# Kernel tuning notes

Measured on AMD Instinct MI355X. Metric: run time of the kernel, lower is better.

Reference implementation:

```python
import jax, jax.numpy as jnp
import numpy as np

SEARCH_RANGE = 4


def setup_inputs() -> dict:
    key = jax.random.key(0)
    k1, k2 = jax.random.split(key)
    B, C, H, W = 4, 64, 256, 256
    x1 = jax.random.normal(k1, (B, C, H, W), dtype=jnp.float32)
    x2 = jax.random.normal(k2, (B, C, H, W), dtype=jnp.float32)
    return {"x1": x1, "x2": x2}


def reference(x1, x2):
    r = SEARCH_RANGE
    D = (2 * r + 1) ** 2
    B, C, H, W = x1.shape
    # zero-pad x2 so out-of-range correlations contribute 0 (matches the
    # original, which leaves those cv entries at their zero init)
    x2p = jnp.pad(x2, ((0, 0), (0, 0), (r, r), (r, r)))
    chans = [None] * D
    for i in range(-r, r + 1):
        for j in range(-r, r + 1):
            # torch cv[:, (2r+1)*i + j] wraps negative indices -> mod D
            k = ((2 * r + 1) * i + j) % D
            # x2 sample at (h - i, w - j): window of padded x2
            win = jax.lax.dynamic_slice(
                x2p, (0, 0, r - i, r - j), (B, C, H, W))
            chans[k] = jnp.sum(x1 * win, axis=1)  # [B,H,W]
    cv = jnp.stack(chans, axis=1)  # [B,D,H,W]
    return jax.nn.softmax(cv, axis=1)  # alpha=1, raw_output=False
```

## Files before the change

### kernel.cpp

```cpp
#include <hip/hip_runtime.h>
#include <stddef.h>

namespace {
constexpr int Hc = 256, Wc = 256, Cc = 64, Bc = 4, Dc = 81;
constexpr int CH = Hc * Wc;
}

#define PIN() asm volatile("" ::: "memory")
#define VMW(N) asm volatile("s_waitcnt vmcnt(" #N ")" ::: "memory")

#define DPPL(x) __builtin_amdgcn_update_dpp(0, (x), 0x138, 0xf, 0xf, true)
#define DPPR(x) __builtin_amdgcn_update_dpp(0, (x), 0x130, 0xf, 0xf, true)

typedef __fp16 half2v __attribute__((ext_vector_type(2)));

static __device__ __forceinline__ int pk2(float a, float b) {
#if __has_builtin(__builtin_amdgcn_cvt_pkrtz)
    half2v h = __builtin_amdgcn_cvt_pkrtz(a, b);
#else
    half2v h; h.x = (__fp16)a; h.y = (__fp16)b;
#endif
    return __builtin_bit_cast(int, h);
}

static __device__ __forceinline__ float dot2f(int q, int w, float c) {
#if __has_builtin(__builtin_amdgcn_fdot2)
    return __builtin_amdgcn_fdot2(__builtin_bit_cast(half2v, q),
                                  __builtin_bit_cast(half2v, w), c, false);
#else
    half2v a = __builtin_bit_cast(half2v, q);
    half2v b = __builtin_bit_cast(half2v, w);
    return c + (float)a.x * (float)b.x + (float)a.y * (float)b.y;
#endif
}

#define FMP(A0, A1, XI)                                                     \
    do {                                                                    \
        const int P0_ = pk2(A0.x, A1.x), P1_ = pk2(A0.y, A1.y);             \
        const int P2_ = pk2(A0.z, A1.z), P3_ = pk2(A0.w, A1.w);             \
        const int w_[12] = {DPPL(P0_), DPPL(P1_), DPPL(P2_), DPPL(P3_),     \
                            P0_,       P1_,       P2_,       P3_,           \
                            DPPR(P0_), DPPR(P1_), DPPR(P2_), DPPR(P3_)};    \
        const int q_[4] = {XI.x, XI.y, XI.z, XI.w};                         \
        _Pragma("unroll") for (int jj = 0; jj < 9; ++jj)                    \
            _Pragma("unroll") for (int s = 0; s < 4; ++s)                   \
                acc[jj][s] = dot2f(q_[s], w_[s - jj + 8], acc[jj][s]);      \
    } while (0)

#define ISX(T, OFF)                                                         \
    do {                                                                    \
        xq##T = *(const float4*)(x2p + (size_t)(OFF) * CH);                 \
        PIN();                                                              \
    } while (0)

#define RX1(X, IDX) X = *(const int4*)&xp[(IDX) * 256 + 4 * t]

__global__ __launch_bounds__(576)
void corr_softmax_kernel(const float* __restrict__ x1,
                         const float* __restrict__ x2,
                         float* __restrict__ out)
{
    __shared__ __align__(16) int xp[32 * 256];

    const int tid = threadIdx.x;
    const int wi  = tid >> 6;
    const int t   = tid & 63;
    const int bid = blockIdx.x;
    const int bh  = (bid & 7) * 128 + (bid >> 3);
    const int b   = bh >> 8;
    const int h   = bh & 255;

    const float* x1row = x1 + (size_t)b * Cc * CH + (size_t)h * Wc;
#pragma unroll
    for (int kk = 0; kk < 4; ++kk) {
        const int T = tid + 576 * kk;
        if (T < 2048) {
            const int e = T >> 6, p = T & 63;
            float4 a0 = *(const float4*)(x1row + (size_t)(2 * e) * CH + 4 * p);
            float4 a1 = *(const float4*)(x1row + (size_t)(2 * e + 1) * CH + 4 * p);
            int4 w;
            w.x = pk2(a0.x, a1.x); w.y = pk2(a0.y, a1.y);
            w.z = pk2(a0.z, a1.z); w.w = pk2(a0.w, a1.w);
            *(int4*)&xp[e * 256 + 4 * p] = w;
        }
    }
    __syncthreads();

    float acc[9][4];
#pragma unroll
    for (int jj = 0; jj < 9; ++jj)
#pragma unroll
        for (int s = 0; s < 4; ++s)
            acc[jj][s] = 0.f;

    const int r  = h + 4 - wi;
    const int rr = (r < 0) ? 0 : ((r > 255) ? 255 : r);

    const float* x2p = x2 + (size_t)b * Cc * CH + (size_t)rr * Wc + 4 * t;

    float4 xq0, xq1, xq2, xq3, xq4, xq5, xq6, xq7;
    int4 xa, xb;

    ISX(0, 0); ISX(1, 1); ISX(2, 2); ISX(3, 3);
    ISX(4, 4); ISX(5, 5); ISX(6, 6); ISX(7, 7);
    RX1(xa, 0);

#pragma unroll 1
    for (int g = 0; g < 7; ++g) {
        const int e1 = 4 * g;
        VMW(6); RX1(xb, e1 + 1); FMP(xq0, xq1, xa); ISX(0, 8);  ISX(1, 9);
        VMW(6); RX1(xa, e1 + 2); FMP(xq2, xq3, xb); ISX(2, 10); ISX(3, 11);
        VMW(6); RX1(xb, e1 + 3); FMP(xq4, xq5, xa); ISX(4, 12); ISX(5, 13);
        VMW(6); RX1(xa, e1 + 4); FMP(xq6, xq7, xb); ISX(6, 14); ISX(7, 15);
        x2p += (size_t)8 * CH;
    }
    VMW(6); RX1(xb, 29); FMP(xq0, xq1, xa);
    VMW(4); RX1(xa, 30); FMP(xq2, xq3, xb);
    VMW(2); RX1(xb, 31); FMP(xq4, xq5, xa);
    VMW(0); FMP(xq6, xq7, xb);

    if ((unsigned)r >= (unsigned)Hc) {
#pragma unroll
        for (int jj = 0; jj < 9; ++jj)
#pragma unroll
            for (int s = 0; s < 4; ++s)
                acc[jj][s] = 0.f;
    }

    __syncthreads();
    float* red = (float*)xp;

    float m0, m1, m2, m3;
    {
        float v0 = acc[0][0], v1 = acc[0][1], v2 = acc[0][2], v3 = acc[0][3];
#pragma unroll
        for (int jj = 1; jj < 9; ++jj) {
            v0 = fmaxf(v0, acc[jj][0]);
            v1 = fmaxf(v1, acc[jj][1]);
            v2 = fmaxf(v2, acc[jj][2]);
            v3 = fmaxf(v3, acc[jj][3]);
        }
        m0 = v0; m1 = v1; m2 = v2; m3 = v3;
    }
    *(float4*)(red + wi * 256 + 4 * t) = make_float4(m0, m1, m2, m3);
    __syncthreads();

    float M0, M1, M2, M3;
    {
        float4 q = *(const float4*)(red + 4 * t);
        M0 = q.x; M1 = q.y; M2 = q.z; M3 = q.w;
#pragma unroll
        for (int w2 = 1; w2 < 9; ++w2) {
            float4 qq = *(const float4*)(red + w2 * 256 + 4 * t);
            M0 = fmaxf(M0, qq.x); M1 = fmaxf(M1, qq.y);
            M2 = fmaxf(M2, qq.z); M3 = fmaxf(M3, qq.w);
        }
    }

    float s0 = 0.f, s1 = 0.f, s2 = 0.f, s3 = 0.f;
#pragma unroll
    for (int jj = 0; jj < 9; ++jj) {
        acc[jj][0] = __expf(acc[jj][0] - M0); s0 += acc[jj][0];
        acc[jj][1] = __expf(acc[jj][1] - M1); s1 += acc[jj][1];
        acc[jj][2] = __expf(acc[jj][2] - M2); s2 += acc[jj][2];
        acc[jj][3] = __expf(acc[jj][3] - M3); s3 += acc[jj][3];
    }
    __syncthreads();
    *(float4*)(red + wi * 256 + 4 * t) = make_float4(s0, s1, s2, s3);
    __syncthreads();

    float S0, S1, S2, S3;
    {
        float4 q = *(const float4*)(red + 4 * t);
        S0 = q.x; S1 = q.y; S2 = q.z; S3 = q.w;
#pragma unroll
        for (int w2 = 1; w2 < 9; ++w2) {
            float4 qq = *(const float4*)(red + w2 * 256 + 4 * t);
            S0 += qq.x; S1 += qq.y; S2 += qq.z; S3 += qq.w;
        }
    }
    const float i0 = 1.0f / S0, i1 = 1.0f / S1, i2 = 1.0f / S2, i3 = 1.0f / S3;

    float* outp = out + (size_t)b * Dc * CH + (size_t)h * Wc + 4 * t;
#pragma unroll
    for (int jj = 0; jj < 9; ++jj) {
        int kc = 9 * wi + jj + 41;
        if (kc >= 81) kc -= 81;
        float4 o = make_float4(acc[jj][0] * i0, acc[jj][1] * i1,
                               acc[jj][2] * i2, acc[jj][3] * i3);
        *(float4*)(outp + (size_t)kc * CH) = o;
    }
}

extern "C" void kernel_launch(void* const* d_in, const int* in_sizes, int n_in,
                              void* d_out, int out_size, void* d_ws, size_t ws_size,
                              hipStream_t stream) {
    (void)in_sizes; (void)n_in; (void)d_ws; (void)ws_size; (void)out_size;
    const float* x1 = (const float*)d_in[0];
    const float* x2 = (const float*)d_in[1];
    float* out = (float*)d_out;
    dim3 grid(Bc * Hc);
    dim3 block(576);
    hipLaunchKernelGGL(corr_softmax_kernel, grid, block, 0, stream, x1, x2, out);
}
```

Baseline: 77.14 us.

## Split each row across two blocks and channel halves per wave with halo exchange

```diff
diff --git a/kernel.cpp b/kernel.cpp
--- a/kernel.cpp
+++ b/kernel.cpp
@@ -8,6 +8,7 @@
 
 #define PIN() asm volatile("" ::: "memory")
 #define VMW(N) asm volatile("s_waitcnt vmcnt(" #N ")" ::: "memory")
+#define LGK(N) asm volatile("s_waitcnt lgkmcnt(" #N ")" ::: "memory")
 
 #define DPPL(x) __builtin_amdgcn_update_dpp(0, (x), 0x138, 0xf, 0xf, true)
 #define DPPR(x) __builtin_amdgcn_update_dpp(0, (x), 0x130, 0xf, 0xf, true)
@@ -34,54 +35,134 @@
 #endif
 }
 
-#define FMP(A0, A1, XI)                                                     \
+#define FMPx(A0, A1, XI, SM, LS)                                            \
     do {                                                                    \
         const int P0_ = pk2(A0.x, A1.x), P1_ = pk2(A0.y, A1.y);             \
         const int P2_ = pk2(A0.z, A1.z), P3_ = pk2(A0.w, A1.w);             \
-        const int w_[12] = {DPPL(P0_), DPPL(P1_), DPPL(P2_), DPPL(P3_),     \
-                            P0_,       P1_,       P2_,       P3_,           \
-                            DPPR(P0_), DPPR(P1_), DPPR(P2_), DPPR(P3_)};    \
+        int l0_ = DPPL(P0_), l1_ = DPPL(P1_);                               \
+        int l2_ = DPPL(P2_), l3_ = DPPL(P3_);                               \
+        int r0_ = DPPR(P0_), r1_ = DPPR(P1_);                               \
+        int r2_ = DPPR(P2_), r3_ = DPPR(P3_);                               \
+        if (LS) {                                                           \
+            l0_ = c0 ? SM.x : l0_; l1_ = c0 ? SM.y : l1_;                   \
+            l2_ = c0 ? SM.z : l2_; l3_ = c0 ? SM.w : l3_;                   \
+            r0_ = c31 ? 0 : r0_;  r1_ = c31 ? 0 : r1_;                      \
+            r2_ = c31 ? 0 : r2_;  r3_ = c31 ? 0 : r3_;                      \
+        } else {                                                            \
+            l0_ = c0 ? 0 : l0_;  l1_ = c0 ? 0 : l1_;                        \
+            l2_ = c0 ? 0 : l2_;  l3_ = c0 ? 0 : l3_;                        \
+            r0_ = c31 ? SM.x : r0_; r1_ = c31 ? SM.y : r1_;                 \
+            r2_ = c31 ? SM.z : r2_; r3_ = c31 ? SM.w : r3_;                 \
+        }                                                                   \
+        const int w_[12] = {l0_, l1_, l2_, l3_, P0_, P1_, P2_, P3_,         \
+                            r0_, r1_, r2_, r3_};                            \
         const int q_[4] = {XI.x, XI.y, XI.z, XI.w};                         \
         _Pragma("unroll") for (int jj = 0; jj < 9; ++jj)                    \
             _Pragma("unroll") for (int s = 0; s < 4; ++s)                   \
                 acc[jj][s] = dot2f(q_[s], w_[s - jj + 8], acc[jj][s]);      \
     } while (0)
 
-#define ISX(T, OFF)                                                         \
-    do {                                                                    \
-        xq##T = *(const float4*)(x2p + (size_t)(OFF) * CH);                 \
+#define STEPF(Qa, Qb, XC, SC, XN, SN, E2, OA, OB, LS)                       \
+    do {                                                                    \
+        VMW(6);                                                             \
+        XN = *(const int4*)&xp[(hb + (E2)) * 128 + 4 * tl];                 \
+        SN = *(const int4*)&smk[4 * (wi * 32 + hb + (E2))];                 \
+        LGK(4);                                                             \
+        FMPx(Qa, Qb, XC, SC, LS);                                           \
+        Qa = *(const float4*)(x2p + (size_t)(OA) * CH);                     \
+        Qb = *(const float4*)(x2p + (size_t)(OB) * CH);                     \
         PIN();                                                              \
     } while (0)
 
-#define RX1(X, IDX) X = *(const int4*)&xp[(IDX) * 256 + 4 * t]
+#define STEPD(Qa, Qb, XC, SC, XN, SN, E2, VN, LS)                           \
+    do {                                                                    \
+        VMW(VN);                                                            \
+        XN = *(const int4*)&xp[(hb + (E2)) * 128 + 4 * tl];                 \
+        SN = *(const int4*)&smk[4 * (wi * 32 + hb + (E2))];                 \
+        LGK(4);                                                             \
+        FMPx(Qa, Qb, XC, SC, LS);                                           \
+    } while (0)
+
+#define STEPZ(Qa, Qb, XC, SC, VN, LN, LS)                                   \
+    do { VMW(VN); LGK(LN); FMPx(Qa, Qb, XC, SC, LS); } while (0)
+
+#define MAINLOOP(LS)                                                        \
+    do {                                                                    \
+        STEPF(xq0, xq1, xiA, smA, xiC, smC, 2, 8, 9, LS);                   \
+        STEPF(xq2, xq3, xiB, smB, xiA, smA, 3, 10, 11, LS);                 \
+        STEPF(xq4, xq5, xiC, smC, xiB, smB, 4, 12, 13, LS);                 \
+        STEPF(xq6, xq7, xiA, smA, xiC, smC, 5, 14, 15, LS);                 \
+        x2p += (size_t)8 * CH;                                              \
+        STEPF(xq0, xq1, xiB, smB, xiA, smA, 6, 8, 9, LS);                   \
+        STEPF(xq2, xq3, xiC, smC, xiB, smB, 7, 10, 11, LS);                 \
+        STEPF(xq4, xq5, xiA, smA, xiC, smC, 8, 12, 13, LS);                 \
+        STEPF(xq6, xq7, xiB, smB, xiA, smA, 9, 14, 15, LS);                 \
+        x2p += (size_t)8 * CH;                                              \
+        STEPF(xq0, xq1, xiC, smC, xiB, smB, 10, 8, 9, LS);                  \
+        STEPF(xq2, xq3, xiA, smA, xiC, smC, 11, 10, 11, LS);                \
+        STEPF(xq4, xq5, xiB, smB, xiA, smA, 12, 12, 13, LS);                \
+        STEPF(xq6, xq7, xiC, smC, xiB, smB, 13, 14, 15, LS);                \
+        x2p += (size_t)8 * CH;                                              \
+        STEPD(xq0, xq1, xiA, smA, xiC, smC, 14, 6, LS);                     \
+        STEPD(xq2, xq3, xiB, smB, xiA, smA, 15, 4, LS);                     \
+        STEPZ(xq4, xq5, xiC, smC, 2, 2, LS);                                \
+        STEPZ(xq6, xq7, xiA, smA, 0, 0, LS);                                \
+    } while (0)
 
 __global__ __launch_bounds__(576)
 void corr_softmax_kernel(const float* __restrict__ x1,
                          const float* __restrict__ x2,
                          float* __restrict__ out)
 {
-    __shared__ __align__(16) int xp[32 * 256];
-
-    const int tid = threadIdx.x;
-    const int wi  = tid >> 6;
-    const int t   = tid & 63;
+    __shared__ __align__(16) int xp[32 * 128];
+    __shared__ __align__(16) int smk[9 * 32 * 4];
+
+    const int tid  = threadIdx.x;
+    const int wi   = tid >> 6;
+    const int t    = tid & 63;
+    const int half = t >> 5;
+    const int tl   = t & 31;
+    const int hb   = 16 * half;
+    const bool c0  = (tl == 0), c31 = (tl == 31);
+
     const int bid = blockIdx.x;
-    const int bh  = (bid & 7) * 128 + (bid >> 3);
-    const int b   = bh >> 8;
-    const int h   = bh & 255;
-
-    const float* x1row = x1 + (size_t)b * Cc * CH + (size_t)h * Wc;
-#pragma unroll
-    for (int kk = 0; kk < 4; ++kk) {
+    const int u   = (bid & 7) * 256 + (bid >> 3);
+    const int b   = u >> 9;
+    const int rem = u & 511;
+    const int h   = rem >> 1;
+    const int hw  = rem & 1;
+
+    const int r  = h + 4 - wi;
+    const int rr = (r < 0) ? 0 : ((r > 255) ? 255 : r);
+
+    const float* x1row = x1 + (size_t)b * Cc * CH + (size_t)h * Wc + 128 * hw;
+#pragma unroll
+    for (int kk = 0; kk < 2; ++kk) {
         const int T = tid + 576 * kk;
-        if (T < 2048) {
-            const int e = T >> 6, p = T & 63;
+        if (T < 1024) {
+            const int e = T >> 5, p = T & 31;
             float4 a0 = *(const float4*)(x1row + (size_t)(2 * e) * CH + 4 * p);
-            float4 a1 = *(const float4*)(x1row + (size_t)(2 * e + 1) * CH + 4 * p);
+            float4 a1 = *(const float4*)(x1row + (size_t)(2 * e) * CH + CH + 4 * p);
             int4 w;
             w.x = pk2(a0.x, a1.x); w.y = pk2(a0.y, a1.y);
             w.z = pk2(a0.z, a1.z); w.w = pk2(a0.w, a1.w);
-            *(int4*)&xp[e * 256 + 4 * p] = w;
+            *(int4*)&xp[e * 128 + 4 * p] = w;
+        }
+    }
+
+    {
+        const int sb = hw ? 124 : 128;
+        const float* sp = x2 + (size_t)b * Cc * CH + (size_t)t * CH
+                        + (size_t)rr * Wc + sb;
+        float4 sv = *(const float4*)sp;
+        float4 pv;
+        pv.x = __shfl_xor(sv.x, 1); pv.y = __shfl_xor(sv.y, 1);
+        pv.z = __shfl_xor(sv.z, 1); pv.w = __shfl_xor(sv.w, 1);
+        if ((t & 1) == 0) {
+            int4 w;
+            w.x = pk2(sv.x, pv.x); w.y = pk2(sv.y, pv.y);
+            w.z = pk2(sv.z, pv.z); w.w = pk2(sv.w, pv.w);
+            *(int4*)&smk[4 * (wi * 32 + (t >> 1))] = w;
         }
     }
     __syncthreads();
@@ -93,31 +174,27 @@
         for (int s = 0; s < 4; ++s)
             acc[jj][s] = 0.f;
 
-    const int r  = h + 4 - wi;
-    const int rr = (r < 0) ? 0 : ((r > 255) ? 255 : r);
-
-    const float* x2p = x2 + (size_t)b * Cc * CH + (size_t)rr * Wc + 4 * t;
+    const float* x2p = x2 + (size_t)b * Cc * CH + (size_t)(32 * half) * CH
+                     + (size_t)rr * Wc + 128 * hw + 4 * tl;
 
     float4 xq0, xq1, xq2, xq3, xq4, xq5, xq6, xq7;
-    int4 xa, xb;
-
-    ISX(0, 0); ISX(1, 1); ISX(2, 2); ISX(3, 3);
-    ISX(4, 4); ISX(5, 5); ISX(6, 6); ISX(7, 7);
-    RX1(xa, 0);
-
-#pragma unroll 1
-    for (int g = 0; g < 7; ++g) {
-        const int e1 = 4 * g;
-        VMW(6); RX1(xb, e1 + 1); FMP(xq0, xq1, xa); ISX(0, 8);  ISX(1, 9);
-        VMW(6); RX1(xa, e1 + 2); FMP(xq2, xq3, xb); ISX(2, 10); ISX(3, 11);
-        VMW(6); RX1(xb, e1 + 3); FMP(xq4, xq5, xa); ISX(4, 12); ISX(5, 13);
-        VMW(6); RX1(xa, e1 + 4); FMP(xq6, xq7, xb); ISX(6, 14); ISX(7, 15);
-        x2p += (size_t)8 * CH;
-    }
-    VMW(6); RX1(xb, 29); FMP(xq0, xq1, xa);
-    VMW(4); RX1(xa, 30); FMP(xq2, xq3, xb);
-    VMW(2); RX1(xb, 31); FMP(xq4, xq5, xa);
-    VMW(0); FMP(xq6, xq7, xb);
+    int4 xiA, xiB, xiC, smA, smB, smC;
+
+    xiA = *(const int4*)&xp[(hb + 0) * 128 + 4 * tl];
+    smA = *(const int4*)&smk[4 * (wi * 32 + hb + 0)];
+    xiB = *(const int4*)&xp[(hb + 1) * 128 + 4 * tl];
+    smB = *(const int4*)&smk[4 * (wi * 32 + hb + 1)];
+    xq0 = *(const float4*)(x2p + (size_t)0 * CH);
+    xq1 = *(const float4*)(x2p + (size_t)1 * CH);
+    xq2 = *(const float4*)(x2p + (size_t)2 * CH);
+    xq3 = *(const float4*)(x2p + (size_t)3 * CH);
+    xq4 = *(const float4*)(x2p + (size_t)4 * CH);
+    xq5 = *(const float4*)(x2p + (size_t)5 * CH);
+    xq6 = *(const float4*)(x2p + (size_t)6 * CH);
+    xq7 = *(const float4*)(x2p + (size_t)7 * CH);
+    PIN();
+
+    if (hw == 0) { MAINLOOP(0); } else { MAINLOOP(1); }
 
     if ((unsigned)r >= (unsigned)Hc) {
 #pragma unroll
@@ -126,6 +203,12 @@
             for (int s = 0; s < 4; ++s)
                 acc[jj][s] = 0.f;
     }
+
+#pragma unroll
+    for (int jj = 0; jj < 9; ++jj)
+#pragma unroll
+        for (int s = 0; s < 4; ++s)
+            acc[jj][s] += __shfl_xor(acc[jj][s], 32);
 
     __syncthreads();
     float* red = (float*)xp;
@@ -142,16 +225,17 @@
         }
         m0 = v0; m1 = v1; m2 = v2; m3 = v3;
     }
-    *(float4*)(red + wi * 256 + 4 * t) = make_float4(m0, m1, m2, m3);
+    if (half == 0)
+        *(float4*)(red + wi * 128 + 4 * tl) = make_float4(m0, m1, m2, m3);
     __syncthreads();
 
     float M0, M1, M2, M3;
     {
-        float4 q = *(const float4*)(red + 4 * t);
+        float4 q = *(const float4*)(red + 4 * tl);
         M0 = q.x; M1 = q.y; M2 = q.z; M3 = q.w;
 #pragma unroll
         for (int w2 = 1; w2 < 9; ++w2) {
-            float4 qq = *(const float4*)(red + w2 * 256 + 4 * t);
+            float4 qq = *(const float4*)(red + w2 * 128 + 4 * tl);
             M0 = fmaxf(M0, qq.x); M1 = fmaxf(M1, qq.y);
             M2 = fmaxf(M2, qq.z); M3 = fmaxf(M3, qq.w);
         }
@@ -166,29 +250,33 @@
         acc[jj][3] = __expf(acc[jj][3] - M3); s3 += acc[jj][3];
     }
     __syncthreads();
-    *(float4*)(red + wi * 256 + 4 * t) = make_float4(s0, s1, s2, s3);
+    if (half == 0)
+        *(float4*)(red + wi * 128 + 4 * tl) = make_float4(s0, s1, s2, s3);
     __syncthreads();
 
     float S0, S1, S2, S3;
     {
-        float4 q = *(const float4*)(red + 4 * t);
+        float4 q = *(const float4*)(red + 4 * tl);
         S0 = q.x; S1 = q.y; S2 = q.z; S3 = q.w;
 #pragma unroll
         for (int w2 = 1; w2 < 9; ++w2) {
-            float4 qq = *(const float4*)(red + w2 * 256 + 4 * t);
+            float4 qq = *(const float4*)(red + w2 * 128 + 4 * tl);
             S0 += qq.x; S1 += qq.y; S2 += qq.z; S3 += qq.w;
         }
     }
     const float i0 = 1.0f / S0, i1 = 1.0f / S1, i2 = 1.0f / S2, i3 = 1.0f / S3;
 
-    float* outp = out + (size_t)b * Dc * CH + (size_t)h * Wc + 4 * t;
-#pragma unroll
-    for (int jj = 0; jj < 9; ++jj) {
-        int kc = 9 * wi + jj + 41;
-        if (kc >= 81) kc -= 81;
-        float4 o = make_float4(acc[jj][0] * i0, acc[jj][1] * i1,
-                               acc[jj][2] * i2, acc[jj][3] * i3);
-        *(float4*)(outp + (size_t)kc * CH) = o;
+    if (half == 0) {
+        float* outp = out + (size_t)b * Dc * CH + (size_t)h * Wc
+                    + 128 * hw + 4 * tl;
+#pragma unroll
+        for (int jj = 0; jj < 9; ++jj) {
+            int kc = 9 * wi + jj + 41;
+            if (kc >= 81) kc -= 81;
+            float4 o = make_float4(acc[jj][0] * i0, acc[jj][1] * i1,
+                                   acc[jj][2] * i2, acc[jj][3] * i3);
+            *(float4*)(outp + (size_t)kc * CH) = o;
+        }
     }
 }
 
@@ -199,7 +287,7 @@
     const float* x1 = (const float*)d_in[0];
     const float* x2 = (const float*)d_in[1];
     float* out = (float*)d_out;
-    dim3 grid(Bc * Hc);
+    dim3 grid(2048);
     dim3 block(576);
     hipLaunchKernelGGL(corr_softmax_kernel, grid, block, 0, stream, x1, x2, out);
 }
```

Result: slower. 98.58 us (+27.8%).

## Process four rows per block with persistent grid and prefetch next x1 row

Applied to the files above, without the earlier changes.

```diff
diff --git a/kernel.cpp b/kernel.cpp
--- a/kernel.cpp
+++ b/kernel.cpp
@@ -55,140 +55,155 @@
 
 #define RX1(X, IDX) X = *(const int4*)&xp[(IDX) * 256 + 4 * t]
 
+#define STAGE_X1(BB, HH)                                                    \
+    do {                                                                    \
+        const float* x1row_ = x1 + (size_t)(BB) * Cc * CH + (size_t)(HH) * Wc; \
+        _Pragma("unroll")                                                   \
+        for (int kk = 0; kk < 4; ++kk) {                                    \
+            const int T = tid + 576 * kk;                                   \
+            if (T < 2048) {                                                 \
+                const int e = T >> 6, p = T & 63;                           \
+                float4 a0 = *(const float4*)(x1row_ + (size_t)(2 * e) * CH + 4 * p); \
+                float4 a1 = *(const float4*)(x1row_ + (size_t)(2 * e + 1) * CH + 4 * p); \
+                int4 w;                                                     \
+                w.x = pk2(a0.x, a1.x); w.y = pk2(a0.y, a1.y);               \
+                w.z = pk2(a0.z, a1.z); w.w = pk2(a0.w, a1.w);               \
+                *(int4*)&xp[e * 256 + 4 * p] = w;                           \
+            }                                                               \
+        }                                                                   \
+    } while (0)
+
 __global__ __launch_bounds__(576)
 void corr_softmax_kernel(const float* __restrict__ x1,
                          const float* __restrict__ x2,
                          float* __restrict__ out)
 {
-    __shared__ __align__(16) int xp[32 * 256];
+    __shared__ __align__(16) int   xp[32 * 256];
+    __shared__ __align__(16) float red[9 * 256];
 
     const int tid = threadIdx.x;
     const int wi  = tid >> 6;
     const int t   = tid & 63;
-    const int bid = blockIdx.x;
-    const int bh  = (bid & 7) * 128 + (bid >> 3);
-    const int b   = bh >> 8;
-    const int h   = bh & 255;
-
-    const float* x1row = x1 + (size_t)b * Cc * CH + (size_t)h * Wc;
-#pragma unroll
-    for (int kk = 0; kk < 4; ++kk) {
-        const int T = tid + 576 * kk;
-        if (T < 2048) {
-            const int e = T >> 6, p = T & 63;
-            float4 a0 = *(const float4*)(x1row + (size_t)(2 * e) * CH + 4 * p);
-            float4 a1 = *(const float4*)(x1row + (size_t)(2 * e + 1) * CH + 4 * p);
-            int4 w;
-            w.x = pk2(a0.x, a1.x); w.y = pk2(a0.y, a1.y);
-            w.z = pk2(a0.z, a1.z); w.w = pk2(a0.w, a1.w);
-            *(int4*)&xp[e * 256 + 4 * p] = w;
-        }
-    }
+    const int bid  = blockIdx.x;
+    const int base = (bid & 7) * 128 + (bid >> 3) * 4;
+
+    STAGE_X1(base >> 8, base & 255);
     __syncthreads();
 
-    float acc[9][4];
-#pragma unroll
-    for (int jj = 0; jj < 9; ++jj)
-#pragma unroll
-        for (int s = 0; s < 4; ++s)
-            acc[jj][s] = 0.f;
-
-    const int r  = h + 4 - wi;
-    const int rr = (r < 0) ? 0 : ((r > 255) ? 255 : r);
-
-    const float* x2p = x2 + (size_t)b * Cc * CH + (size_t)rr * Wc + 4 * t;
-
-    float4 xq0, xq1, xq2, xq3, xq4, xq5, xq6, xq7;
-    int4 xa, xb;
-
-    ISX(0, 0); ISX(1, 1); ISX(2, 2); ISX(3, 3);
-    ISX(4, 4); ISX(5, 5); ISX(6, 6); ISX(7, 7);
-    RX1(xa, 0);
-
 #pragma unroll 1
-    for (int g = 0; g < 7; ++g) {
-        const int e1 = 4 * g;
-        VMW(6); RX1(xb, e1 + 1); FMP(xq0, xq1, xa); ISX(0, 8);  ISX(1, 9);
-        VMW(6); RX1(xa, e1 + 2); FMP(xq2, xq3, xb); ISX(2, 10); ISX(3, 11);
-        VMW(6); RX1(xb, e1 + 3); FMP(xq4, xq5, xa); ISX(4, 12); ISX(5, 13);
-        VMW(6); RX1(xa, e1 + 4); FMP(xq6, xq7, xb); ISX(6, 14); ISX(7, 15);
-        x2p += (size_t)8 * CH;
-    }
-    VMW(6); RX1(xb, 29); FMP(xq0, xq1, xa);
-    VMW(4); RX1(xa, 30); FMP(xq2, xq3, xb);
-    VMW(2); RX1(xb, 31); FMP(xq4, xq5, xa);
-    VMW(0); FMP(xq6, xq7, xb);
-
-    if ((unsigned)r >= (unsigned)Hc) {
+    for (int it4 = 0; it4 < 4; ++it4) {
+        const int bh = base + it4;
+        const int b  = bh >> 8;
+        const int h  = bh & 255;
+
+        float acc[9][4];
 #pragma unroll
         for (int jj = 0; jj < 9; ++jj)
 #pragma unroll
             for (int s = 0; s < 4; ++s)
                 acc[jj][s] = 0.f;
-    }
-
-    __syncthreads();
-    float* red = (float*)xp;
-
-    float m0, m1, m2, m3;
-    {
-        float v0 = acc[0][0], v1 = acc[0][1], v2 = acc[0][2], v3 = acc[0][3];
-#pragma unroll
-        for (int jj = 1; jj < 9; ++jj) {
-            v0 = fmaxf(v0, acc[jj][0]);
-            v1 = fmaxf(v1, acc[jj][1]);
-            v2 = fmaxf(v2, acc[jj][2]);
-            v3 = fmaxf(v3, acc[jj][3]);
-        }
-        m0 = v0; m1 = v1; m2 = v2; m3 = v3;
-    }
-    *(float4*)(red + wi * 256 + 4 * t) = make_float4(m0, m1, m2, m3);
-    __syncthreads();
-
-    float M0, M1, M2, M3;
-    {
-        float4 q = *(const float4*)(red + 4 * t);
-        M0 = q.x; M1 = q.y; M2 = q.z; M3 = q.w;
-#pragma unroll
-        for (int w2 = 1; w2 < 9; ++w2) {
-            float4 qq = *(const float4*)(red + w2 * 256 + 4 * t);
-            M0 = fmaxf(M0, qq.x); M1 = fmaxf(M1, qq.y);
-            M2 = fmaxf(M2, qq.z); M3 = fmaxf(M3, qq.w);
-        }
-    }
-
-    float s0 = 0.f, s1 = 0.f, s2 = 0.f, s3 = 0.f;
-#pragma unroll
-    for (int jj = 0; jj < 9; ++jj) {
-        acc[jj][0] = __expf(acc[jj][0] - M0); s0 += acc[jj][0];
-        acc[jj][1] = __expf(acc[jj][1] - M1); s1 += acc[jj][1];
-        acc[jj][2] = __expf(acc[jj][2] - M2); s2 += acc[jj][2];
-        acc[jj][3] = __expf(acc[jj][3] - M3); s3 += acc[jj][3];
-    }
-    __syncthreads();
-    *(float4*)(red + wi * 256 + 4 * t) = make_float4(s0, s1, s2, s3);
-    __syncthreads();
-
-    float S0, S1, S2, S3;
-    {
-        float4 q = *(const float4*)(red + 4 * t);
-        S0 = q.x; S1 = q.y; S2 = q.z; S3 = q.w;
-#pragma unroll
-        for (int w2 = 1; w2 < 9; ++w2) {
-            float4 qq = *(const float4*)(red + w2 * 256 + 4 * t);
-            S0 += qq.x; S1 += qq.y; S2 += qq.z; S3 += qq.w;
-        }
-    }
-    const float i0 = 1.0f / S0, i1 = 1.0f / S1, i2 = 1.0f / S2, i3 = 1.0f / S3;
-
-    float* outp = out + (size_t)b * Dc * CH + (size_t)h * Wc + 4 * t;
-#pragma unroll
-    for (int jj = 0; jj < 9; ++jj) {
-        int kc = 9 * wi + jj + 41;
-        if (kc >= 81) kc -= 81;
-        float4 o = make_float4(acc[jj][0] * i0, acc[jj][1] * i1,
-                               acc[jj][2] * i2, acc[jj][3] * i3);
-        *(float4*)(outp + (size_t)kc * CH) = o;
+
+        const int r  = h + 4 - wi;
+        const int rr = (r < 0) ? 0 : ((r > 255) ? 255 : r);
+
+        const float* x2p = x2 + (size_t)b * Cc * CH + (size_t)rr * Wc + 4 * t;
+
+        float4 xq0, xq1, xq2, xq3, xq4, xq5, xq6, xq7;
+        int4 xa, xb;
+
+        ISX(0, 0); ISX(1, 1); ISX(2, 2); ISX(3, 3);
+        ISX(4, 4); ISX(5, 5); ISX(6, 6); ISX(7, 7);
+        RX1(xa, 0);
+
+#pragma unroll 1
+        for (int g = 0; g < 7; ++g) {
+            const int e1 = 4 * g;
+            VMW(6); RX1(xb, e1 + 1); FMP(xq0, xq1, xa); ISX(0, 8);  ISX(1, 9);
+            VMW(6); RX1(xa, e1 + 2); FMP(xq2, xq3, xb); ISX(2, 10); ISX(3, 11);
+            VMW(6); RX1(xb, e1 + 3); FMP(xq4, xq5, xa); ISX(4, 12); ISX(5, 13);
+            VMW(6); RX1(xa, e1 + 4); FMP(xq6, xq7, xb); ISX(6, 14); ISX(7, 15);
+            x2p += (size_t)8 * CH;
+        }
+        VMW(6); RX1(xb, 29); FMP(xq0, xq1, xa);
+        VMW(4); RX1(xa, 30); FMP(xq2, xq3, xb);
+        VMW(2); RX1(xb, 31); FMP(xq4, xq5, xa);
+        VMW(0); FMP(xq6, xq7, xb);
+
+        if ((unsigned)r >= (unsigned)Hc) {
+#pragma unroll
+            for (int jj = 0; jj < 9; ++jj)
+#pragma unroll
+                for (int s = 0; s < 4; ++s)
+                    acc[jj][s] = 0.f;
+        }
+
+        __syncthreads();
+
+        if (it4 < 3) {
+            const int bh2 = base + it4 + 1;
+            STAGE_X1(bh2 >> 8, bh2 & 255);
+        }
+
+        float m0, m1, m2, m3;
+        {
+            float v0 = acc[0][0], v1 = acc[0][1], v2 = acc[0][2], v3 = acc[0][3];
+#pragma unroll
+            for (int jj = 1; jj < 9; ++jj) {
+                v0 = fmaxf(v0, acc[jj][0]);
+                v1 = fmaxf(v1, acc[jj][1]);
+                v2 = fmaxf(v2, acc[jj][2]);
+                v3 = fmaxf(v3, acc[jj][3]);
+            }
+            m0 = v0; m1 = v1; m2 = v2; m3 = v3;
+        }
+        *(float4*)(red + wi * 256 + 4 * t) = make_float4(m0, m1, m2, m3);
+        __syncthreads();
+
+        float M0, M1, M2, M3;
+        {
+            float4 q = *(const float4*)(red + 4 * t);
+            M0 = q.x; M1 = q.y; M2 = q.z; M3 = q.w;
+#pragma unroll
+            for (int w2 = 1; w2 < 9; ++w2) {
+                float4 qq = *(const float4*)(red + w2 * 256 + 4 * t);
+                M0 = fmaxf(M0, qq.x); M1 = fmaxf(M1, qq.y);
+                M2 = fmaxf(M2, qq.z); M3 = fmaxf(M3, qq.w);
+            }
+        }
+
+        float s0 = 0.f, s1 = 0.f, s2 = 0.f, s3 = 0.f;
+#pragma unroll
+        for (int jj = 0; jj < 9; ++jj) {
+            acc[jj][0] = __expf(acc[jj][0] - M0); s0 += acc[jj][0];
+            acc[jj][1] = __expf(acc[jj][1] - M1); s1 += acc[jj][1];
+            acc[jj][2] = __expf(acc[jj][2] - M2); s2 += acc[jj][2];
+            acc[jj][3] = __expf(acc[jj][3] - M3); s3 += acc[jj][3];
+        }
+        __syncthreads();
+        *(float4*)(red + wi * 256 + 4 * t) = make_float4(s0, s1, s2, s3);
+        __syncthreads();
+
+        float S0, S1, S2, S3;
+        {
+            float4 q = *(const float4*)(red + 4 * t);
+            S0 = q.x; S1 = q.y; S2 = q.z; S3 = q.w;
+#pragma unroll
+            for (int w2 = 1; w2 < 9; ++w2) {
+                float4 qq = *(const float4*)(red + w2 * 256 + 4 * t);
+                S0 += qq.x; S1 += qq.y; S2 += qq.z; S3 += qq.w;
+            }
+        }
+        const float i0 = 1.f/S0, i1 = 1.f/S1, i2 = 1.f/S2, i3 = 1.f/S3;
+
+        float* outp = out + (size_t)b * Dc * CH + (size_t)h * Wc + 4 * t;
+#pragma unroll
+        for (int jj = 0; jj < 9; ++jj) {
+            int kc = 9 * wi + jj + 41;
+            if (kc >= 81) kc -= 81;
+            float4 o = make_float4(acc[jj][0] * i0, acc[jj][1] * i1,
+                                   acc[jj][2] * i2, acc[jj][3] * i3);
+            *(float4*)(outp + (size_t)kc * CH) = o;
+        }
     }
 }
 
@@ -199,7 +214,7 @@
     const float* x1 = (const float*)d_in[0];
     const float* x2 = (const float*)d_in[1];
     float* out = (float*)d_out;
-    dim3 grid(Bc * Hc);
+    dim3 grid(256);
     dim3 block(576);
     hipLaunchKernelGGL(corr_softmax_kernel, grid, block, 0, stream, x1, x2, out);
 }
```

Result: slower. 86.79 us (+12.5%).
